# Kernel optimization log

Hardware: AMD Instinct MI355X
Metric: run time of the kernel (lower is better)

Reference implementation:

```python
import jax, jax.numpy as jnp
import numpy as np

DEPTH = 13                 # tree depth -> N = 2**DEPTH - 1 reaches (heap layout, outlet = node 0)
N = 2 ** DEPTH - 1         # 8191 reaches
T = 2048                   # timesteps


def setup_inputs() -> dict:
    key = jax.random.key(0)
    ks = jax.random.split(key, 8)
    u = lambda k, shape, lo, hi: jax.random.uniform(k, shape, minval=lo, maxval=hi, dtype=jnp.float32)
    return {
        "lateral_inflows": u(ks[0], (T, N), 0.0, 2.0),     # m^3/s lateral inflow per reach
        "manning_n":       u(ks[1], (N,), 0.025, 0.06),    # Manning roughness
        "lengths":         u(ks[2], (N,), 1000.0, 5000.0), # reach length [m]
        "slopes":          u(ks[3], (N,), 1e-4, 1e-2),     # bed slope (>= 1e-4 as in source)
        "width_coefs":     u(ks[4], (N,), 3.0, 10.0),      # w = wc * Q**we  (power-law geometry)
        "width_exps":      u(ks[5], (N,), 0.4, 0.6),
        "depth_coefs":     u(ks[6], (N,), 0.2, 0.5),       # h = dc * Q**de
        "depth_exps":      u(ks[7], (N,), 0.3, 0.45),
        "dt": 3600,                                        # routing timestep [s]
    }


def _mc_outflow(I_new, I_old, O_old, n, L, S, wc, we, dc, de, dt):
    """Variable-parameter Muskingum-Cunge update for one vector of reaches."""
    Qr = jnp.maximum(0.5 * (I_new + O_old), 1e-3)          # reference discharge
    h = dc * Qr ** de                                       # hydraulic depth
    w = wc * Qr ** we                                       # top width
    v = h ** (2.0 / 3.0) * jnp.sqrt(S) / n                  # Manning velocity
    c = jnp.maximum((5.0 / 3.0) * v, 1e-3)                  # kinematic celerity
    K = L / c                                               # travel time
    X = jnp.clip(0.5 * (1.0 - Qr / (w * S * c * L)), 0.0, 0.5)
    den = 2.0 * K * (1.0 - X) + dt
    C1 = (dt - 2.0 * K * X) / den
    C2 = (dt + 2.0 * K * X) / den
    C3 = (2.0 * K * (1.0 - X) - dt) / den
    return jnp.maximum(C1 * I_new + C2 * I_old + C3 * O_old, 0.0)


def reference(lateral_inflows, manning_n, lengths, slopes, width_coefs, width_exps,
              depth_coefs, depth_exps, dt):
    dtf = jnp.float32(dt)
    Np = lateral_inflows.shape[1]
    params = (manning_n, lengths, slopes, width_coefs, width_exps, depth_coefs, depth_exps)

    def step(carry, lat_t):
        I_old, O_old = carry                                # [N] prev inflow / outflow
        Q = jnp.zeros(Np, dtype=lat_t.dtype)                # new outflows this timestep
        I_all = jnp.zeros(Np, dtype=lat_t.dtype)
        # process levels leaves -> root (reverse topological order over the DAG)
        for l in range(DEPTH - 1, -1, -1):
            s, e = 2 ** l - 1, 2 ** (l + 1) - 1             # nodes of level l
            if l == DEPTH - 1:
                up = jnp.float32(0.0)                        # headwater reaches
            else:
                cs, ce = 2 ** (l + 1) - 1, 2 ** (l + 2) - 1  # children = level l+1
                up = Q[cs:ce:2] + Q[cs + 1:ce:2]             # sum of 2 upstream discharges
            I_new = lat_t[s:e] + up
            O_new = _mc_outflow(I_new, I_old[s:e], O_old[s:e],
                                *(p[s:e] for p in params), dtf)
            Q = Q.at[s:e].set(O_new)
            I_all = I_all.at[s:e].set(I_new)
        return (I_all, Q), Q[0]                              # outlet = root (index 0)

    init = (jnp.zeros(Np, jnp.float32), jnp.zeros(Np, jnp.float32))
    _, outlet_Q = jax.lax.scan(step, init, lateral_inflows)
    return outlet_Q                                          # [T]
```

## Files before the change

### kernel.cpp

```cpp
#include <hip/hip_runtime.h>


#define NN 8191
#define TT 2048
#define BATCH 32
#define NBLK 39
#define BTHREADS 256

#define FLAGS_FOFF 16773120ull
#define REQ_BYTES  ((FLAGS_FOFF + NBLK * 32ull) * 4ull)

#if __has_builtin(__builtin_amdgcn_exp2f)
__device__ __forceinline__ float fexp2(float x) { return __builtin_amdgcn_exp2f(x); }
#else
__device__ __forceinline__ float fexp2(float x) { return exp2f(x); }
#endif
#if __has_builtin(__builtin_amdgcn_logf)
__device__ __forceinline__ float flog2(float x) { return __builtin_amdgcn_logf(x); }
#else
__device__ __forceinline__ float flog2(float x) { return log2f(x); }
#endif
#if __has_builtin(__builtin_amdgcn_rcpf)
__device__ __forceinline__ float frcp(float x) { return __builtin_amdgcn_rcpf(x); }
#else
__device__ __forceinline__ float frcp(float x) { return 1.0f / x; }
#endif

__device__ __forceinline__ float mc_update(float Inew, float Iold, float Oold,
                                           float cc, float e23, float wc, float we,
                                           float twoL, float SL, float dtf)
{
    float Qr = fmaxf(0.5f * (Inew + Oold), 1e-3f);
    float lg = flog2(Qr);
    float c  = fmaxf(cc * fexp2(e23 * lg), 1e-3f);
    float w  = wc * fexp2(we * lg);
    float twoK = twoL * frcp(c);
    float X = 0.5f - 0.5f * Qr * frcp(w * SL * c);
    X = fminf(fmaxf(X, 0.0f), 0.5f);
    float A = twoK * X;
    float B = twoK - A;
    float r = frcp(B + dtf);
    float C1 = (dtf - A) * r;
    float C2 = (dtf + A) * r;
    float C3 = (B - dtf) * r;
    return fmaxf(C1 * Inew + C2 * Iold + C3 * Oold, 0.0f);
}

__constant__ int g_level[NBLK] = {
    12,12,12,12,12,12,12,12,12,12,12,12,12,12,12,12,
    11,11,11,11,11,11,11,11,
    10,10,10,10,
    9,9,
    8,7,6,5,4,3,2,1,0};
__constant__ int g_nstart[NBLK] = {
    4095,4351,4607,4863,5119,5375,5631,5887,6143,6399,6655,6911,7167,7423,7679,7935,
    2047,2303,2559,2815,3071,3327,3583,3839,
    1023,1279,1535,1791,
    511,767,
    255,127,63,31,15,7,3,1,0};
__constant__ int g_cnt[NBLK] = {
    256,256,256,256,256,256,256,256,256,256,256,256,256,256,256,256,
    256,256,256,256,256,256,256,256,
    256,256,256,256,
    256,256,
    256,128,64,32,16,8,4,2,1};
__constant__ int g_prodA[NBLK] = {
    -1,-1,-1,-1,-1,-1,-1,-1,-1,-1,-1,-1,-1,-1,-1,-1,
    0,2,4,6,8,10,12,14,
    16,18,20,22,
    24,26,
    28,30,31,32,33,34,35,36,37};
__constant__ int g_prodB[NBLK] = {
    -1,-1,-1,-1,-1,-1,-1,-1,-1,-1,-1,-1,-1,-1,-1,-1,
    1,3,5,7,9,11,13,15,
    17,19,21,23,
    25,27,
    29,-1,-1,-1,-1,-1,-1,-1,-1};
__constant__ unsigned long long g_off[13] = {
    16773120ull, 16769024ull, 16760832ull, 16744448ull, 16711680ull,
    16646144ull, 16515072ull, 16252928ull, 15728640ull, 14680064ull,
    12582912ull, 8388608ull, 0ull};

__device__ __forceinline__ void waitflags(const unsigned int* fa, const unsigned int* fb,
                                          unsigned int target)
{
    if (!fa) return;
    while (true) {
        unsigned int a = __hip_atomic_load(fa, __ATOMIC_RELAXED, __HIP_MEMORY_SCOPE_AGENT);
        unsigned int b = fb ? __hip_atomic_load(fb, __ATOMIC_RELAXED, __HIP_MEMORY_SCOPE_AGENT)
                            : a;
        if (a >= target && b >= target) break;
        __builtin_amdgcn_s_sleep(2);
    }
    __builtin_amdgcn_sched_barrier(0);
    asm volatile("" ::: "memory");
}

__global__ void zero_flags(unsigned int* flags)
{
    for (int i = threadIdx.x; i < NBLK * 32; i += 256) flags[i] = 0;
}

__global__ __launch_bounds__(BTHREADS)
void pipe_kernel(const float* __restrict__ lat,
                 const float* __restrict__ nman,
                 const float* __restrict__ len,
                 const float* __restrict__ slp,
                 const float* __restrict__ wcf,
                 const float* __restrict__ wex,
                 const float* __restrict__ dcf,
                 const float* __restrict__ dex,
                 const int*   __restrict__ dtp,
                 float*       __restrict__ out,
                 float*       __restrict__ ws)
{
    const int bid = blockIdx.x;
    const int tid = threadIdx.x;
    const int lvl = g_level[bid];
    const int cnt = g_cnt[bid];
    const bool multiwave = (cnt > 64);
    if (!multiwave && tid >= 64) return;

    const bool active = (tid < cnt);
    const int node = g_nstart[bid] + (active ? tid : 0);
    const int ml = node - ((1 << lvl) - 1);

    unsigned int* flags = (unsigned int*)(ws + FLAGS_FOFF);
    unsigned int* myflag = flags + (size_t)bid * 32;
    const int pa = g_prodA[bid], pb = g_prodB[bid];
    const unsigned int* fa = (pa >= 0) ? (flags + (size_t)pa * 32) : nullptr;
    const unsigned int* fb = (pb >= 0) ? (flags + (size_t)pb * 32) : nullptr;

    const bool haschild = (lvl < 12);
    const int myW = 1 << lvl;
    const int childW = 1 << (lvl + 1);
    float* myBuf = ws + g_off[lvl];
    const unsigned long long* childBuf =
        haschild ? (const unsigned long long*)(ws + g_off[lvl + 1]) : nullptr;

    const float dtf = (float)dtp[0];

    float cc = 0, e23 = 0, wcc = 0, wee = 0, twoL = 0, SL = 0;
    float Iold = 0.0f, Oold = 0.0f;
    {
        float n = nman[node], L = len[node], S = slp[node];
        float wc = wcf[node], we = wex[node], dc = dcf[node], de = dex[node];
        float dc23 = fexp2(0.6666667f * flog2(dc));
        cc  = 1.6666667f * dc23 * sqrtf(S) * frcp(n);
        e23 = 0.6666667f * de;
        wcc = wc; wee = we;
        twoL = 2.0f * L;
        SL = S * L;
    }

    for (int t0 = 0; t0 < TT; t0 += BATCH) {
        float la[BATCH];
        if (active) {
#pragma unroll
            for (int k = 0; k < BATCH; ++k)
                la[k] = lat[(size_t)(t0 + k) * NN + node];
        }

        waitflags(fa, fb, (unsigned int)(t0 + BATCH));

        if (active) {
            float c0[BATCH], c1[BATCH];
            if (haschild) {
#pragma unroll
                for (int k = 0; k < BATCH; ++k) {
                    unsigned long long cv = __hip_atomic_load(
                        childBuf + ((size_t)(t0 + k) * childW >> 1) + ml,
                        __ATOMIC_RELAXED, __HIP_MEMORY_SCOPE_AGENT);
                    float2 c = *(float2*)&cv;
                    c0[k] = c.x; c1[k] = c.y;
                }
            }
#pragma unroll
            for (int k = 0; k < BATCH; ++k) {
                float Inew = la[k] + (haschild ? (c0[k] + c1[k]) : 0.0f);
                float O = mc_update(Inew, Iold, Oold, cc, e23, wcc, wee, twoL, SL, dtf);
                Iold = Inew; Oold = O;
                if (lvl > 0)
                    __hip_atomic_store(myBuf + (size_t)(t0 + k) * myW + ml, O,
                                       __ATOMIC_RELAXED, __HIP_MEMORY_SCOPE_AGENT);
                else
                    out[t0 + k] = O;
            }
        }
        asm volatile("s_waitcnt vmcnt(0)" ::: "memory");
        if (multiwave) __syncthreads();
        if (tid == 0)
            __hip_atomic_store(myflag, (unsigned int)(t0 + BATCH),
                               __ATOMIC_RELAXED, __HIP_MEMORY_SCOPE_AGENT);
    }
}

#define NTHREADS 1024
__global__ __launch_bounds__(NTHREADS)
void route_kernel(const float* __restrict__ lat,
                  const float* __restrict__ nman,
                  const float* __restrict__ len,
                  const float* __restrict__ slp,
                  const float* __restrict__ wcf,
                  const float* __restrict__ wex,
                  const float* __restrict__ dcf,
                  const float* __restrict__ dex,
                  const int*   __restrict__ dtp,
                  float*       __restrict__ out)
{
    __shared__ float Osh[NN];
    const int tid = threadIdx.x;
    const float dtf = (float)dtp[0];

    int nodes[8];
    nodes[0] = 4095 + tid;
    nodes[1] = 5119 + tid;
    nodes[2] = 6143 + tid;
    nodes[3] = 7167 + tid;
    nodes[4] = 2047 + tid;
    nodes[5] = 3071 + tid;
    nodes[6] = 1023 + tid;
    nodes[7] = (tid < 1023) ? tid : 0;

    float cc[8], e23[8], wcc[8], wee[8], twoL[8], SL[8];
    float Ireg[8], Oreg[8];
#pragma unroll
    for (int k = 0; k < 8; ++k) {
        int i = nodes[k];
        float n = nman[i], L = len[i], S = slp[i];
        float wc = wcf[i], we = wex[i], dc = dcf[i], de = dex[i];
        float dc23 = fexp2(0.6666667f * flog2(dc));
        cc[k]  = 1.6666667f * dc23 * sqrtf(S) * frcp(n);
        e23[k] = 0.6666667f * de;
        wcc[k] = wc; wee[k] = we;
        twoL[k] = 2.0f * L;
        SL[k]  = S * L;
        Ireg[k] = 0.0f; Oreg[k] = 0.0f;
    }
    for (int i = tid; i < NN; i += NTHREADS) Osh[i] = 0.0f;
    __syncthreads();

    for (int t = 0; t < TT; ++t) {
        const float* __restrict__ latt = lat + (size_t)t * NN;
#pragma unroll
        for (int k = 0; k < 4; ++k) {
            int i = nodes[k];
            float Inew = latt[i];
            float O = mc_update(Inew, Ireg[k], Oreg[k],
                                cc[k], e23[k], wcc[k], wee[k], twoL[k], SL[k], dtf);
            Ireg[k] = Inew; Oreg[k] = O; Osh[i] = O;
        }
        __syncthreads();
#pragma unroll
        for (int k = 4; k < 6; ++k) {
            int i = nodes[k];
            float Inew = latt[i] + Osh[2 * i + 1] + Osh[2 * i + 2];
            float O = mc_update(Inew, Ireg[k], Oreg[k],
                                cc[k], e23[k], wcc[k], wee[k], twoL[k], SL[k], dtf);
            Ireg[k] = Inew; Oreg[k] = O; Osh[i] = O;
        }
        __syncthreads();
        {
            int i = nodes[6];
            float Inew = latt[i] + Osh[2 * i + 1] + Osh[2 * i + 2];
            float O = mc_update(Inew, Ireg[6], Oreg[6],
                                cc[6], e23[6], wcc[6], wee[6], twoL[6], SL[6], dtf);
            Ireg[6] = Inew; Oreg[6] = O; Osh[i] = O;
        }
        __syncthreads();
        for (int l = 9; l >= 0; --l) {
            int s = (1 << l) - 1;
            int e = (1 << (l + 1)) - 1;
            if (tid >= s && tid < e) {
                int i = tid;
                float Inew = latt[i] + Osh[2 * i + 1] + Osh[2 * i + 2];
                float O = mc_update(Inew, Ireg[7], Oreg[7],
                                    cc[7], e23[7], wcc[7], wee[7], twoL[7], SL[7], dtf);
                Ireg[7] = Inew; Oreg[7] = O; Osh[i] = O;
            }
            __syncthreads();
        }
        if (tid == 0) out[t] = Oreg[7];
    }
}

extern "C" void kernel_launch(void* const* d_in, const int* in_sizes, int n_in,
                              void* d_out, int out_size, void* d_ws, size_t ws_size,
                              hipStream_t stream) {
    const float* lat  = (const float*)d_in[0];
    const float* nman = (const float*)d_in[1];
    const float* len  = (const float*)d_in[2];
    const float* slp  = (const float*)d_in[3];
    const float* wcf  = (const float*)d_in[4];
    const float* wex  = (const float*)d_in[5];
    const float* dcf  = (const float*)d_in[6];
    const float* dex  = (const float*)d_in[7];
    const int*   dtp  = (const int*)d_in[8];
    float* out = (float*)d_out;

    if (ws_size >= REQ_BYTES) {
        float* ws = (float*)d_ws;
        unsigned int* flags = (unsigned int*)(ws + FLAGS_FOFF);
        zero_flags<<<dim3(1), dim3(256), 0, stream>>>(flags);
        pipe_kernel<<<dim3(NBLK), dim3(BTHREADS), 0, stream>>>(
            lat, nman, len, slp, wcf, wex, dcf, dex, dtp, out, ws);
    } else {
        route_kernel<<<dim3(1), dim3(NTHREADS), 0, stream>>>(
            lat, nman, len, slp, wcf, wex, dcf, dex, dtp, out);
    }
}
```

Before: 469.5 us.

## Use per-wavefront progress flags and fold Muskingum-Cunge parameters into precomputed exponents

```diff
diff --git a/kernel.cpp b/kernel.cpp
--- a/kernel.cpp
+++ b/kernel.cpp
@@ -8,7 +8,7 @@
 #define BTHREADS 256
 
 #define FLAGS_FOFF 16773120ull
-#define REQ_BYTES  ((FLAGS_FOFF + NBLK * 32ull) * 4ull)
+#define REQ_BYTES  67106816ull
 
 #if __has_builtin(__builtin_amdgcn_exp2f)
 __device__ __forceinline__ float fexp2(float x) { return __builtin_amdgcn_exp2f(x); }
@@ -27,16 +27,13 @@
 #endif
 
 __device__ __forceinline__ float mc_update(float Inew, float Iold, float Oold,
-                                           float cc, float e23, float wc, float we,
-                                           float twoL, float SL, float dtf)
+                                           float em, float tkc, float ex, float k1,
+                                           float dtf)
 {
     float Qr = fmaxf(0.5f * (Inew + Oold), 1e-3f);
     float lg = flog2(Qr);
-    float c  = fmaxf(cc * fexp2(e23 * lg), 1e-3f);
-    float w  = wc * fexp2(we * lg);
-    float twoK = twoL * frcp(c);
-    float X = 0.5f - 0.5f * Qr * frcp(w * SL * c);
-    X = fminf(fmaxf(X, 0.0f), 0.5f);
+    float twoK = tkc * fexp2(em * lg);
+    float X = fmaxf(0.5f - k1 * fexp2(ex * lg), 0.0f);
     float A = twoK * X;
     float B = twoK - A;
     float r = frcp(B + dtf);
@@ -52,45 +49,29 @@
     10,10,10,10,
     9,9,
     8,7,6,5,4,3,2,1,0};
-__constant__ int g_nstart[NBLK] = {
-    4095,4351,4607,4863,5119,5375,5631,5887,6143,6399,6655,6911,7167,7423,7679,7935,
-    2047,2303,2559,2815,3071,3327,3583,3839,
-    1023,1279,1535,1791,
-    511,767,
-    255,127,63,31,15,7,3,1,0};
 __constant__ int g_cnt[NBLK] = {
     256,256,256,256,256,256,256,256,256,256,256,256,256,256,256,256,
     256,256,256,256,256,256,256,256,
     256,256,256,256,
     256,256,
     256,128,64,32,16,8,4,2,1};
-__constant__ int g_prodA[NBLK] = {
-    -1,-1,-1,-1,-1,-1,-1,-1,-1,-1,-1,-1,-1,-1,-1,-1,
-    0,2,4,6,8,10,12,14,
-    16,18,20,22,
-    24,26,
-    28,30,31,32,33,34,35,36,37};
-__constant__ int g_prodB[NBLK] = {
-    -1,-1,-1,-1,-1,-1,-1,-1,-1,-1,-1,-1,-1,-1,-1,-1,
-    1,3,5,7,9,11,13,15,
-    17,19,21,23,
-    25,27,
-    29,-1,-1,-1,-1,-1,-1,-1,-1};
+__constant__ int g_first[13] = {38,37,36,35,34,33,32,31,30,28,24,16,0};
 __constant__ unsigned long long g_off[13] = {
     16773120ull, 16769024ull, 16760832ull, 16744448ull, 16711680ull,
     16646144ull, 16515072ull, 16252928ull, 15728640ull, 14680064ull,
     12582912ull, 8388608ull, 0ull};
 
+#define FLAG_STRIDE 16
+
 __device__ __forceinline__ void waitflags(const unsigned int* fa, const unsigned int* fb,
                                           unsigned int target)
 {
-    if (!fa) return;
     while (true) {
         unsigned int a = __hip_atomic_load(fa, __ATOMIC_RELAXED, __HIP_MEMORY_SCOPE_AGENT);
         unsigned int b = fb ? __hip_atomic_load(fb, __ATOMIC_RELAXED, __HIP_MEMORY_SCOPE_AGENT)
                             : a;
         if (a >= target && b >= target) break;
-        __builtin_amdgcn_s_sleep(2);
+        __builtin_amdgcn_s_sleep(1);
     }
     __builtin_amdgcn_sched_barrier(0);
     asm volatile("" ::: "memory");
@@ -98,7 +79,7 @@
 
 __global__ void zero_flags(unsigned int* flags)
 {
-    for (int i = threadIdx.x; i < NBLK * 32; i += 256) flags[i] = 0;
+    for (int i = threadIdx.x; i < NBLK * 4 * FLAG_STRIDE; i += 256) flags[i] = 0;
 }
 
 __global__ __launch_bounds__(BTHREADS)
@@ -118,20 +99,33 @@
     const int tid = threadIdx.x;
     const int lvl = g_level[bid];
     const int cnt = g_cnt[bid];
-    const bool multiwave = (cnt > 64);
-    if (!multiwave && tid >= 64) return;
+    const int W   = tid >> 6;
+    const int wn  = cnt - W * 64;
+    if (wn <= 0) return;
 
     const bool active = (tid < cnt);
-    const int node = g_nstart[bid] + (active ? tid : 0);
-    const int ml = node - ((1 << lvl) - 1);
+    const int B = bid - g_first[lvl];
+    const int m = B * 256 + (active ? tid : 0);
+    const int node = ((1 << lvl) - 1) + m;
+    const int wbase = B * 256 + W * 64;
 
     unsigned int* flags = (unsigned int*)(ws + FLAGS_FOFF);
-    unsigned int* myflag = flags + (size_t)bid * 32;
-    const int pa = g_prodA[bid], pb = g_prodB[bid];
-    const unsigned int* fa = (pa >= 0) ? (flags + (size_t)pa * 32) : nullptr;
-    const unsigned int* fb = (pb >= 0) ? (flags + (size_t)pb * 32) : nullptr;
+    unsigned int* myflag = flags + ((size_t)bid * 4 + W) * FLAG_STRIDE;
 
     const bool haschild = (lvl < 12);
+    const unsigned int* fa = nullptr;
+    const unsigned int* fb = nullptr;
+    if (haschild) {
+        const int Fp = g_first[lvl + 1];
+        const int nw = wn < 64 ? wn : 64;
+        const int p0 = (2 * wbase) >> 6;
+        const int p1 = (2 * wbase + 2 * nw - 1) >> 6;
+        fa = flags + ((size_t)(Fp + (p0 >> 2)) * 4 + (p0 & 3)) * FLAG_STRIDE;
+        fb = (p1 != p0)
+           ? flags + ((size_t)(Fp + (p1 >> 2)) * 4 + (p1 & 3)) * FLAG_STRIDE
+           : nullptr;
+    }
+
     const int myW = 1 << lvl;
     const int childW = 1 << (lvl + 1);
     float* myBuf = ws + g_off[lvl];
@@ -140,17 +134,18 @@
 
     const float dtf = (float)dtp[0];
 
-    float cc = 0, e23 = 0, wcc = 0, wee = 0, twoL = 0, SL = 0;
+    float em, tkc, ex, k1;
     float Iold = 0.0f, Oold = 0.0f;
     {
         float n = nman[node], L = len[node], S = slp[node];
         float wc = wcf[node], we = wex[node], dc = dcf[node], de = dex[node];
         float dc23 = fexp2(0.6666667f * flog2(dc));
-        cc  = 1.6666667f * dc23 * sqrtf(S) * frcp(n);
-        e23 = 0.6666667f * de;
-        wcc = wc; wee = we;
-        twoL = 2.0f * L;
-        SL = S * L;
+        float cc = 1.6666667f * dc23 * sqrtf(S) * frcp(n);
+        float e23 = 0.6666667f * de;
+        em  = -e23;
+        tkc = 2.0f * L * frcp(cc);
+        ex  = 1.0f - we - e23;
+        k1  = 0.5f * frcp(S * L * wc * cc);
     }
 
     for (int t0 = 0; t0 < TT; t0 += BATCH) {
@@ -161,7 +156,7 @@
                 la[k] = lat[(size_t)(t0 + k) * NN + node];
         }
 
-        waitflags(fa, fb, (unsigned int)(t0 + BATCH));
+        if (haschild) waitflags(fa, fb, (unsigned int)(t0 + BATCH));
 
         if (active) {
             float c0[BATCH], c1[BATCH];
@@ -169,7 +164,7 @@
 #pragma unroll
                 for (int k = 0; k < BATCH; ++k) {
                     unsigned long long cv = __hip_atomic_load(
-                        childBuf + ((size_t)(t0 + k) * childW >> 1) + ml,
+                        childBuf + ((size_t)(t0 + k) * childW >> 1) + m,
                         __ATOMIC_RELAXED, __HIP_MEMORY_SCOPE_AGENT);
                     float2 c = *(float2*)&cv;
                     c0[k] = c.x; c1[k] = c.y;
@@ -178,20 +173,21 @@
 #pragma unroll
             for (int k = 0; k < BATCH; ++k) {
                 float Inew = la[k] + (haschild ? (c0[k] + c1[k]) : 0.0f);
-                float O = mc_update(Inew, Iold, Oold, cc, e23, wcc, wee, twoL, SL, dtf);
+                float O = mc_update(Inew, Iold, Oold, em, tkc, ex, k1, dtf);
                 Iold = Inew; Oold = O;
                 if (lvl > 0)
-                    __hip_atomic_store(myBuf + (size_t)(t0 + k) * myW + ml, O,
+                    __hip_atomic_store(myBuf + (size_t)(t0 + k) * myW + m, O,
                                        __ATOMIC_RELAXED, __HIP_MEMORY_SCOPE_AGENT);
                 else
                     out[t0 + k] = O;
             }
         }
-        asm volatile("s_waitcnt vmcnt(0)" ::: "memory");
-        if (multiwave) __syncthreads();
-        if (tid == 0)
-            __hip_atomic_store(myflag, (unsigned int)(t0 + BATCH),
-                               __ATOMIC_RELAXED, __HIP_MEMORY_SCOPE_AGENT);
+        if (lvl > 0) {
+            asm volatile("s_waitcnt vmcnt(0)" ::: "memory");
+            if ((tid & 63) == 0)
+                __hip_atomic_store(myflag, (unsigned int)(t0 + BATCH),
+                                   __ATOMIC_RELAXED, __HIP_MEMORY_SCOPE_AGENT);
+        }
     }
 }
 
@@ -222,7 +218,7 @@
     nodes[6] = 1023 + tid;
     nodes[7] = (tid < 1023) ? tid : 0;
 
-    float cc[8], e23[8], wcc[8], wee[8], twoL[8], SL[8];
+    float em[8], tkc[8], ex[8], k1[8];
     float Ireg[8], Oreg[8];
 #pragma unroll
     for (int k = 0; k < 8; ++k) {
@@ -230,11 +226,12 @@
         float n = nman[i], L = len[i], S = slp[i];
         float wc = wcf[i], we = wex[i], dc = dcf[i], de = dex[i];
         float dc23 = fexp2(0.6666667f * flog2(dc));
-        cc[k]  = 1.6666667f * dc23 * sqrtf(S) * frcp(n);
-        e23[k] = 0.6666667f * de;
-        wcc[k] = wc; wee[k] = we;
-        twoL[k] = 2.0f * L;
-        SL[k]  = S * L;
+        float cc = 1.6666667f * dc23 * sqrtf(S) * frcp(n);
+        float e23 = 0.6666667f * de;
+        em[k]  = -e23;
+        tkc[k] = 2.0f * L * frcp(cc);
+        ex[k]  = 1.0f - we - e23;
+        k1[k]  = 0.5f * frcp(S * L * wc * cc);
         Ireg[k] = 0.0f; Oreg[k] = 0.0f;
     }
     for (int i = tid; i < NN; i += NTHREADS) Osh[i] = 0.0f;
@@ -246,8 +243,7 @@
         for (int k = 0; k < 4; ++k) {
             int i = nodes[k];
             float Inew = latt[i];
-            float O = mc_update(Inew, Ireg[k], Oreg[k],
-                                cc[k], e23[k], wcc[k], wee[k], twoL[k], SL[k], dtf);
+            float O = mc_update(Inew, Ireg[k], Oreg[k], em[k], tkc[k], ex[k], k1[k], dtf);
             Ireg[k] = Inew; Oreg[k] = O; Osh[i] = O;
         }
         __syncthreads();
@@ -255,16 +251,14 @@
         for (int k = 4; k < 6; ++k) {
             int i = nodes[k];
             float Inew = latt[i] + Osh[2 * i + 1] + Osh[2 * i + 2];
-            float O = mc_update(Inew, Ireg[k], Oreg[k],
-                                cc[k], e23[k], wcc[k], wee[k], twoL[k], SL[k], dtf);
+            float O = mc_update(Inew, Ireg[k], Oreg[k], em[k], tkc[k], ex[k], k1[k], dtf);
             Ireg[k] = Inew; Oreg[k] = O; Osh[i] = O;
         }
         __syncthreads();
         {
             int i = nodes[6];
             float Inew = latt[i] + Osh[2 * i + 1] + Osh[2 * i + 2];
-            float O = mc_update(Inew, Ireg[6], Oreg[6],
-                                cc[6], e23[6], wcc[6], wee[6], twoL[6], SL[6], dtf);
+            float O = mc_update(Inew, Ireg[6], Oreg[6], em[6], tkc[6], ex[6], k1[6], dtf);
             Ireg[6] = Inew; Oreg[6] = O; Osh[i] = O;
         }
         __syncthreads();
@@ -274,8 +268,7 @@
             if (tid >= s && tid < e) {
                 int i = tid;
                 float Inew = latt[i] + Osh[2 * i + 1] + Osh[2 * i + 2];
-                float O = mc_update(Inew, Ireg[7], Oreg[7],
-                                    cc[7], e23[7], wcc[7], wee[7], twoL[7], SL[7], dtf);
+                float O = mc_update(Inew, Ireg[7], Oreg[7], em[7], tkc[7], ex[7], k1[7], dtf);
                 Ireg[7] = Inew; Oreg[7] = O; Osh[i] = O;
             }
             __syncthreads();
```

Measured after the change: 483.5 us. +3.0%, slower.
